# Performance work log

Hardware: AMD Instinct MI355X
Metric: run time of the kernel (lower is better)

Reference implementation:

```python
import jax, jax.numpy as jnp
import numpy as np

B, S1, S2, D1, D2 = 4, 2048, 2048, 512, 512
H, DK, DV = 8, 64, 64


def setup_inputs() -> dict:
    key = jax.random.key(0)
    ks = jax.random.split(key, 8)
    x1 = jax.random.normal(ks[0], (B, S1, D1), dtype=jnp.float32)
    x2 = jax.random.normal(ks[1], (B, S2, D2), dtype=jnp.float32)
    x3 = jax.random.normal(ks[2], (B, S2, D2), dtype=jnp.float32)
    s = 0.02
    Wq = jax.random.normal(ks[3], (D1, H * DK), dtype=jnp.float32) * s
    Wk = jax.random.normal(ks[4], (D2, H * DK), dtype=jnp.float32) * s
    Wv = jax.random.normal(ks[5], (D2, H * DV), dtype=jnp.float32) * s
    Wo = jax.random.normal(ks[6], (H * DV, D1), dtype=jnp.float32) * s
    bo = jnp.zeros((D1,), dtype=jnp.float32)
    return {"x1": x1, "x2": x2, "x3": x3, "Wq": Wq, "Wk": Wk, "Wv": Wv, "Wo": Wo, "bo": bo}


def reference(x1, x2, x3, Wq, Wk, Wv, Wo, bo):
    b, s1, _ = x1.shape
    # project to per-head q, k, v: [B, H, S, Dh]
    q = (x1 @ Wq).reshape(b, s1, H, DK).transpose(0, 2, 1, 3)
    k = (x2 @ Wk).reshape(b, x2.shape[1], H, DK).transpose(0, 2, 1, 3)
    v = (x3 @ Wv).reshape(b, x3.shape[1], H, DV).transpose(0, 2, 1, 3)
    scores = jnp.einsum('bhqd,bhkd->bhqk', q, k) / jnp.sqrt(jnp.float32(DK))
    attn = jax.nn.softmax(scores, axis=-1)
    out = jnp.einsum('bhqk,bhkd->bhqd', attn, v)  # [B, H, S1, DV]
    out = out.transpose(0, 2, 1, 3).reshape(b, s1, H * DV)
    return out @ Wo + bo
```

## Files before the change

### kernel.cpp

```cpp
#include <hip/hip_runtime.h>

typedef __attribute__((ext_vector_type(4))) float f32x4;
typedef __attribute__((ext_vector_type(16))) float f32x16;
typedef __attribute__((ext_vector_type(8))) __bf16 bf16x8;
typedef __attribute__((ext_vector_type(4))) __bf16 bf16x4;
typedef __attribute__((ext_vector_type(2))) __bf16 bf16x2;
typedef __attribute__((ext_vector_type(4))) unsigned u32x4;

#define DEVINL __device__ __forceinline__

DEVINL void gld16(const void* g, void* l) {
  __builtin_amdgcn_global_load_lds((__attribute__((address_space(1))) void*)(void*)g,
                                   (__attribute__((address_space(3))) void*)l, 16, 0, 0);
}


__global__ __launch_bounds__(256) void cvt_all(const float* x1, const float* x2, const float* x3,
                                               const float* Wq, const float* Wk, const float* Wv,
                                               const float* Wo, __bf16* o0, __bf16* o1, __bf16* o2,
                                               __bf16* WT) {
  __shared__ float t[64][65];
  const int bx = blockIdx.x;
  if (bx < 12288) {
    const int z = bx >> 12;
    const float* s = z == 0 ? x1 : z == 1 ? x2 : x3;
    __bf16* d = z == 0 ? o0 : z == 1 ? o1 : o2;
    size_t i = (size_t)(bx & 4095) * 256 + threadIdx.x;
    f32x4 v = ((const f32x4*)s)[i];
    bf16x4 o;
#pragma unroll
    for (int j = 0; j < 4; ++j) o[j] = (__bf16)v[j];
    ((bf16x4*)d)[i] = o;
  } else {
    const int l = bx - 12288;
    const int z = l >> 6;
    const float* W = z == 0 ? Wq : z == 1 ? Wk : z == 2 ? Wv : Wo;
    __bf16* D = WT + (size_t)z * 512 * 512;
    const int r0 = ((l >> 3) & 7) * 64, c0 = (l & 7) * 64;
    const int tx = threadIdx.x & 63, ty = threadIdx.x >> 6;
#pragma unroll
    for (int j = 0; j < 16; ++j)
      t[ty + j * 4][tx] = W[(size_t)(r0 + ty + j * 4) * 512 + c0 + tx];
    __syncthreads();
#pragma unroll
    for (int j = 0; j < 16; ++j)
      D[(size_t)(c0 + ty + j * 4) * 512 + r0 + tx] = (__bf16)t[tx][ty + j * 4];
  }
}


DEVINL void gemm_tile(const __bf16* A, const __bf16* Bt, int m0, int n0,
                      __bf16* As, __bf16* Bs, f32x4 acc[4][4]) {
  const int tid = threadIdx.x, lane = tid & 63, w = tid >> 6;
  const int qd = lane >> 4, r = lane & 15;
  const int wm = w & 1, wn = w >> 1;
  const char* ap[4];
  const char* bp[4];
#pragma unroll
  for (int j = 0; j < 4; ++j) {
    int c = (w * 4 + j) * 64 + lane;
    int row = c >> 3, cs = c & 7;
    int gc = cs ^ (row & 7);
    ap[j] = (const char*)A + (size_t)(m0 + row) * 1024 + gc * 16;
    bp[j] = (const char*)Bt + (size_t)(n0 + row) * 1024 + gc * 16;
  }
  int offA[4][2], offB[4][2];
#pragma unroll
  for (int t = 0; t < 4; ++t)
#pragma unroll
    for (int ks = 0; ks < 2; ++ks) {
      int m = wm * 64 + t * 16 + r;
      offA[t][ks] = m * 128 + (((ks * 4 + qd) ^ (m & 7)) * 16);
      int n = wn * 64 + t * 16 + r;
      offB[t][ks] = n * 128 + (((ks * 4 + qd) ^ (n & 7)) * 16);
    }
  char* AsC = (char*)As;
  char* BsC = (char*)Bs;
  for (int kt = 0; kt < 8; ++kt) {
    __syncthreads();
#pragma unroll
    for (int j = 0; j < 4; ++j) {
      gld16(ap[j] + kt * 128, AsC + (w * 4 + j) * 1024);
      gld16(bp[j] + kt * 128, BsC + (w * 4 + j) * 1024);
    }
    __syncthreads();
#pragma unroll
    for (int ks = 0; ks < 2; ++ks) {
      bf16x8 a[4], b[4];
#pragma unroll
      for (int t = 0; t < 4; ++t) {
        a[t] = *(const bf16x8*)(AsC + offA[t][ks]);
        b[t] = *(const bf16x8*)(BsC + offB[t][ks]);
      }
#pragma unroll
      for (int i = 0; i < 4; ++i)
#pragma unroll
        for (int j2 = 0; j2 < 4; ++j2)
          acc[i][j2] = __builtin_amdgcn_mfma_f32_16x16x32_bf16(a[i], b[j2], acc[i][j2], 0, 0, 0);
    }
  }
}

__global__ __launch_bounds__(256, 3) void gemm_proj(const __bf16* x1b, const __bf16* x2b,
                                                    const __bf16* x3b, const __bf16* WT,
                                                    __bf16* Qo, __bf16* Ko, __bf16* Vto) {
  __shared__ __align__(16) char smem[34816];
  __bf16* As = (__bf16*)smem;
  __bf16* Bs = (__bf16*)(smem + 16384);
  const int z = blockIdx.z;
  const __bf16* A = z == 0 ? x1b : z == 1 ? x2b : x3b;
  const __bf16* Bt = WT + (size_t)z * 512 * 512;
  const int l = blockIdx.x;
  const int sidx = l >> 3;
  const int m0 = ((l & 7) * 8 + (sidx >> 2)) * 128;
  const int n0 = (sidx & 3) * 128;
  f32x4 acc[4][4] = {};
  gemm_tile(A, Bt, m0, n0, As, Bs, acc);
  const int tid = threadIdx.x, lane = tid & 63, w = tid >> 6;
  const int qd = lane >> 4, r = lane & 15, wm = w & 1, wn = w >> 1;
  const int b = m0 >> 11, sbase = m0 & 2047;
  if (z == 2) {
    __syncthreads();
    char* T = smem;
#pragma unroll
    for (int mt = 0; mt < 4; ++mt)
#pragma unroll
      for (int nt = 0; nt < 4; ++nt) {
        int dv = wn * 64 + nt * 16 + r;
        int sl = wm * 64 + mt * 16 + qd * 4;
        bf16x4 p4;
#pragma unroll
        for (int g = 0; g < 4; ++g) p4[g] = (__bf16)acc[mt][nt][g];
        *(bf16x4*)(T + (size_t)dv * 272 + sl * 2) = p4;
      }
    __syncthreads();
#pragma unroll
    for (int p2 = 0; p2 < 2; ++p2) {
      int dvrow = p2 * 64 + (tid >> 2);
      int col = n0 + dvrow, h = col >> 6, d = col & 63;
      __bf16* dst = Vto + ((size_t)(b * 8 + h) * 64 + d) * 2048 + sbase + (tid & 3) * 8;
#pragma unroll
      for (int j = 0; j < 4; ++j) {
        bf16x8 vv = *(const bf16x8*)(T + (size_t)dvrow * 272 + (tid & 3) * 16 + j * 64);
        *(bf16x8*)(dst + j * 32) = vv;
      }
    }
  } else {
    const float qscale = 0.18033688f;
#pragma unroll
    for (int mt = 0; mt < 4; ++mt) {
#pragma unroll
      for (int nt = 0; nt < 4; ++nt) {
        f32x4 v = acc[mt][nt];
        if (z == 0) {
#pragma unroll
          for (int g = 0; g < 4; ++g) v[g] *= qscale;
        }
        int col = n0 + wn * 64 + nt * 16 + r;
        int h = col >> 6, d = col & 63;
        int s = sbase + wm * 64 + mt * 16 + qd * 4;
        __bf16* O = (z == 0 ? Qo : Ko) + ((size_t)(b * 8 + h) * 2048 + s) * 64 + d;
#pragma unroll
        for (int g = 0; g < 4; ++g) O[(size_t)g * 64] = (__bf16)v[g];
      }
    }
  }
}

__global__ __launch_bounds__(256, 2) void gemm_out(const __bf16* Op, const float* Lp,
                                                   const __bf16* WoT, const float* bo,
                                                   float* out) {
  __shared__ __align__(16) __bf16 As[64 * 64];
  __shared__ __align__(16) __bf16 Bs[128 * 64];
  const int tid = threadIdx.x, lane = tid & 63, w = tid >> 6;
  const int qd = lane >> 4, r = lane & 15, wm = w & 1, wn = w >> 1;
  const int id = blockIdx.x;
  const int rest = id >> 3;
  const int m0 = ((id & 7) * 16 + (rest & 15)) * 64;
  const int n0 = (rest >> 4) * 128;
  const int b8 = (m0 >> 11) * 8;
  const int sb = m0 & 2047;
  const char* bp[4];
#pragma unroll
  for (int j = 0; j < 4; ++j) {
    int c = (w * 4 + j) * 64 + lane;
    int row = c >> 3, gc = (c & 7) ^ (row & 7);
    bp[j] = (const char*)WoT + (size_t)(n0 + row) * 1024 + gc * 16;
  }
  int arow[2], ach[2];
#pragma unroll
  for (int j = 0; j < 2; ++j) {
    int c = (w * 2 + j) * 64 + lane;
    arow[j] = c >> 3;
    ach[j] = c & 7;
  }
  int offA[2][2], offB[4][2];
#pragma unroll
  for (int ks = 0; ks < 2; ++ks) {
#pragma unroll
    for (int t = 0; t < 2; ++t) {
      int m = wm * 32 + t * 16 + r;
      offA[t][ks] = m * 128 + (((ks * 4 + qd) ^ (m & 7)) * 16);
    }
#pragma unroll
    for (int t = 0; t < 4; ++t) {
      int n = wn * 64 + t * 16 + r;
      offB[t][ks] = n * 128 + (((ks * 4 + qd) ^ (n & 7)) * 16);
    }
  }
  char* AsC = (char*)As;
  char* BsC = (char*)Bs;
  bf16x8 pa0[2], pa1[2];
  float pinv[2];
  auto loadA = [&](int h) {
#pragma unroll
    for (int j = 0; j < 2; ++j) {
      size_t rr = (size_t)(b8 + h) * 2048 + sb + arow[j];
      const __bf16* p0 = Op + rr * 64 + ach[j] * 8;
      pa0[j] = *(const bf16x8*)p0;
      pa1[j] = *(const bf16x8*)(p0 + (size_t)32 * 2048 * 64);
      pinv[j] = 1.0f / (Lp[rr] + Lp[rr + 65536]);
    }
  };
  loadA(0);
  f32x4 acc[2][4] = {};
  for (int kt = 0; kt < 8; ++kt) {
    __syncthreads();
#pragma unroll
    for (int j = 0; j < 4; ++j) gld16(bp[j] + kt * 128, BsC + (w * 4 + j) * 1024);
#pragma unroll
    for (int j = 0; j < 2; ++j) {
      bf16x8 q;
#pragma unroll
      for (int k2 = 0; k2 < 8; ++k2)
        q[k2] = (__bf16)(((float)pa0[j][k2] + (float)pa1[j][k2]) * pinv[j]);
      *(bf16x8*)(AsC + arow[j] * 128 + (ach[j] ^ (arow[j] & 7)) * 16) = q;
    }
    __syncthreads();
    if (kt < 7) loadA(kt + 1);
#pragma unroll
    for (int ks = 0; ks < 2; ++ks) {
      bf16x8 a[2], b[4];
#pragma unroll
      for (int t = 0; t < 2; ++t) a[t] = *(const bf16x8*)(AsC + offA[t][ks]);
#pragma unroll
      for (int t = 0; t < 4; ++t) b[t] = *(const bf16x8*)(BsC + offB[t][ks]);
#pragma unroll
      for (int i = 0; i < 2; ++i)
#pragma unroll
        for (int j2 = 0; j2 < 4; ++j2)
          acc[i][j2] = __builtin_amdgcn_mfma_f32_16x16x32_bf16(a[i], b[j2], acc[i][j2], 0, 0, 0);
    }
  }
#pragma unroll
  for (int nt = 0; nt < 4; ++nt) {
    int col = n0 + wn * 64 + nt * 16 + r;
    float bv = bo[col];
#pragma unroll
    for (int mt = 0; mt < 2; ++mt) {
      int mg = m0 + wm * 32 + mt * 16 + qd * 4;
#pragma unroll
      for (int g = 0; g < 4; ++g) out[(size_t)(mg + g) * 512 + col] = acc[mt][nt][g] + bv;
    }
  }
}

__global__ __launch_bounds__(256, 4) void attn(const __bf16* Q, const __bf16* K,
                                               const __bf16* Vt, __bf16* Opart, float* Lp) {
  __shared__ __align__(16) __bf16 Qs[128 * 64];
  __shared__ __align__(16) __bf16 Ksd[2][64 * 64];
  __shared__ __align__(16) __bf16 Vs[64 * 64];
  const int tid = threadIdx.x, lane = tid & 63, w = tid >> 6;
  const int l31 = lane & 31, lh = lane >> 5;
  const int id = blockIdx.x;
  const int rest = id >> 3;
  const int bh = (id & 7) * 4 + (rest >> 5);
  const int kvh = (rest >> 4) & 1;
  const int q0 = (rest & 15) * 128;
  const __bf16* Qg = Q + ((size_t)bh * 2048 + q0) * 64;
  const __bf16* Kg = K + (size_t)bh * 2048 * 64;
  const __bf16* Vg = Vt + (size_t)bh * 64 * 2048;
  char* QsC = (char*)Qs;
  char* Ks0 = (char*)Ksd;
  char* Ks1 = (char*)Ksd + 8192;
  char* VsC = (char*)Vs;

  const char* Kst[2];
  const char* Vst[2];
  int ldso[2];
#pragma unroll
  for (int j = 0; j < 2; ++j) {
    int c = (w * 2 + j) * 64 + lane;
    int m = c >> 3, gc = (c & 7) ^ (m & 7);
    int ms = (m & ~12) | ((m & 4) << 1) | ((m & 8) >> 1);
    Kst[j] = (const char*)Kg + (size_t)ms * 128 + gc * 16;
    Vst[j] = (const char*)Vg + (size_t)m * 4096 + gc * 16;
    ldso[j] = (w * 2 + j) * 1024;
  }

  const int kt0 = kvh * 16;

#pragma unroll
  for (int j = 0; j < 4; ++j) {
    int c = (w * 4 + j) * 64 + lane;
    int m = c >> 3, gc = (c & 7) ^ (m & 7);
    gld16((const char*)Qg + m * 128 + gc * 16, QsC + (w * 4 + j) * 1024);
  }
#pragma unroll
  for (int j = 0; j < 2; ++j) gld16(Kst[j] + (size_t)kt0 * 8192, Ks0 + ldso[j]);
  asm volatile("s_waitcnt vmcnt(0)" ::: "memory");
  __builtin_amdgcn_sched_barrier(0);
  __builtin_amdgcn_s_barrier();
  __builtin_amdgcn_sched_barrier(0);

  const int rb = l31 * 128;
  const int he = (((lane & 7) ^ lh) << 4);

  bf16x8 qf[4];
#pragma unroll
  for (int c = 0; c < 4; ++c)
    qf[c] = *(const bf16x8*)(QsC + (w * 32 + l31) * 128 + ((c << 5) ^ he));

  bf16x8 ones;
#pragma unroll
  for (int j = 0; j < 8; ++j) ones[j] = (__bf16)1.0f;

  f32x16 oacc[2] = {};
  f32x16 lacc = {};

  auto iter = [&](int kt, int ktn, char* Kc, char* Kn) {
    gld16(Vst[0] + (size_t)kt * 128, VsC + ldso[0]);
    gld16(Vst[1] + (size_t)kt * 128, VsC + ldso[1]);
    gld16(Kst[0] + (size_t)ktn * 8192, Kn + ldso[0]);
    gld16(Kst[1] + (size_t)ktn * 8192, Kn + ldso[1]);
    __builtin_amdgcn_sched_barrier(0);

    unsigned pk[2][8];
#pragma unroll
    for (int t2 = 0; t2 < 2; ++t2) {
      f32x16 s = {};
      __builtin_amdgcn_s_setprio(1);
#pragma unroll
      for (int c = 0; c < 4; ++c) {
        bf16x8 kf = *(const bf16x8*)(Kc + t2 * 4096 + rb + ((c << 5) ^ he));
        s = __builtin_amdgcn_mfma_f32_32x32x16_bf16(kf, qf[c], s, 0, 0, 0);
      }
      __builtin_amdgcn_s_setprio(0);
#pragma unroll
      for (int i = 0; i < 8; ++i) {
        bf16x2 t;
        t[0] = (__bf16)__builtin_exp2f(s[2 * i]);
        t[1] = (__bf16)__builtin_exp2f(s[2 * i + 1]);
        pk[t2][i] = __builtin_bit_cast(unsigned, t);
      }
    }
    bf16x8 pa[4];
#pragma unroll
    for (int c = 0; c < 4; ++c) {
      u32x4 u = {pk[c >> 1][(c & 1) * 4 + 0], pk[c >> 1][(c & 1) * 4 + 1],
                 pk[c >> 1][(c & 1) * 4 + 2], pk[c >> 1][(c & 1) * 4 + 3]};
      pa[c] = __builtin_bit_cast(bf16x8, u);
    }

    asm volatile("s_waitcnt vmcnt(2)" ::: "memory");
    __builtin_amdgcn_sched_barrier(0);
    __builtin_amdgcn_s_barrier();
    __builtin_amdgcn_sched_barrier(0);

    __builtin_amdgcn_s_setprio(1);
#pragma unroll
    for (int c = 0; c < 4; ++c) {
      lacc = __builtin_amdgcn_mfma_f32_32x32x16_bf16(pa[c], ones, lacc, 0, 0, 0);
#pragma unroll
      for (int dvt = 0; dvt < 2; ++dvt) {
        bf16x8 vf = *(const bf16x8*)(VsC + dvt * 4096 + rb + ((c << 5) ^ he));
        oacc[dvt] = __builtin_amdgcn_mfma_f32_32x32x16_bf16(pa[c], vf, oacc[dvt], 0, 0, 0);
      }
    }
    __builtin_amdgcn_s_setprio(0);

    asm volatile("s_waitcnt vmcnt(0)" ::: "memory");
    __builtin_amdgcn_sched_barrier(0);
    __builtin_amdgcn_s_barrier();
    __builtin_amdgcn_sched_barrier(0);
  };

#pragma unroll 1
  for (int kt = kt0; kt < kt0 + 16; kt += 2) {
    iter(kt, kt + 1, Ks0, Ks1);
    int kt2 = (kt + 2 < kt0 + 16) ? kt + 2 : kt + 1;
    iter(kt + 1, kt2, Ks1, Ks0);
  }

  const size_t pbase = (size_t)(kvh * 32 + bh) * 2048;
  if (l31 == 0) {
#pragma unroll
    for (int g = 0; g < 16; ++g)
      Lp[pbase + q0 + w * 32 + (g & 3) + 8 * (g >> 2) + 4 * lh] = lacc[g];
  }
  __bf16* Ob0 = Opart + pbase * 64;
#pragma unroll
  for (int dvt = 0; dvt < 2; ++dvt) {
#pragma unroll
    for (int g = 0; g < 16; ++g) {
      int s = q0 + w * 32 + (g & 3) + 8 * (g >> 2) + 4 * lh;
      Ob0[(size_t)s * 64 + dvt * 32 + l31] = (__bf16)oacc[dvt][g];
    }
  }
}


extern "C" void kernel_launch(void* const* d_in, const int* in_sizes, int n_in,
                              void* d_out, int out_size, void* d_ws, size_t ws_size,
                              hipStream_t stream) {
  const float* x1 = (const float*)d_in[0];
  const float* x2 = (const float*)d_in[1];
  const float* x3 = (const float*)d_in[2];
  const float* Wq = (const float*)d_in[3];
  const float* Wk = (const float*)d_in[4];
  const float* Wv = (const float*)d_in[5];
  const float* Wo = (const float*)d_in[6];
  const float* bo = (const float*)d_in[7];
  float* out = (float*)d_out;
  char* ws = (char*)d_ws;
  const size_t MB = 1ull << 20;
  __bf16* x1b = (__bf16*)(ws);
  __bf16* x2b = (__bf16*)(ws + 8 * MB);
  __bf16* x3b = (__bf16*)(ws + 16 * MB);
  __bf16* WT = (__bf16*)(ws + 24 * MB);
  __bf16* Qb = (__bf16*)(ws + 26 * MB);
  __bf16* Kb = (__bf16*)(ws + 34 * MB);
  __bf16* Vtb = (__bf16*)(ws + 42 * MB);
  __bf16* Opart = (__bf16*)(ws + 58 * MB);
  float* Lp = (float*)(ws + 74 * MB);

  cvt_all<<<dim3(12544), 256, 0, stream>>>(x1, x2, x3, Wq, Wk, Wv, Wo, x1b, x2b, x3b, WT);
  gemm_proj<<<dim3(256, 1, 3), 256, 0, stream>>>(x1b, x2b, x3b, WT, Qb, Kb, Vtb);
  attn<<<dim3(1024), 256, 0, stream>>>(Qb, Kb, Vtb, Opart, Lp);
  gemm_out<<<dim3(512), 256, 0, stream>>>(Opart, Lp, WT + 3ull * 512 * 512, bo, out);
}
```

Before: 194.3 us.

## Software-pipeline attention loop: overlap next QK and softmax with current PV

```diff
diff --git a/kernel.cpp b/kernel.cpp
--- a/kernel.cpp
+++ b/kernel.cpp
@@ -277,49 +277,50 @@
   const int bh = (id & 7) * 4 + (rest >> 5);
   const int kvh = (rest >> 4) & 1;
   const int q0 = (rest & 15) * 128;
-  const __bf16* Qg = Q + ((size_t)bh * 2048 + q0) * 64;
-  const __bf16* Kg = K + (size_t)bh * 2048 * 64;
-  const __bf16* Vg = Vt + (size_t)bh * 64 * 2048;
+  const char* QgC = (const char*)(Q + ((size_t)bh * 2048 + q0) * 64);
+  const char* KgC = (const char*)(K + (size_t)bh * 2048 * 64);
+  const char* VgC = (const char*)(Vt + (size_t)bh * 64 * 2048);
   char* QsC = (char*)Qs;
-  char* Ks0 = (char*)Ksd;
-  char* Ks1 = (char*)Ksd + 8192;
   char* VsC = (char*)Vs;
-
-  const char* Kst[2];
-  const char* Vst[2];
-  int ldso[2];
+  char* Kc = (char*)Ksd;
+  char* Kn = (char*)Ksd + 8192;
+
+  int koff[2], voff[2], ldso[2];
 #pragma unroll
   for (int j = 0; j < 2; ++j) {
     int c = (w * 2 + j) * 64 + lane;
     int m = c >> 3, gc = (c & 7) ^ (m & 7);
     int ms = (m & ~12) | ((m & 4) << 1) | ((m & 8) >> 1);
-    Kst[j] = (const char*)Kg + (size_t)ms * 128 + gc * 16;
-    Vst[j] = (const char*)Vg + (size_t)m * 4096 + gc * 16;
+    koff[j] = ms * 128 + gc * 16;
+    voff[j] = m * 4096 + gc * 16;
     ldso[j] = (w * 2 + j) * 1024;
   }
 
   const int kt0 = kvh * 16;
+  const size_t kb = (size_t)kt0 * 8192;
+  const size_t vb = (size_t)kt0 * 128;
 
 #pragma unroll
   for (int j = 0; j < 4; ++j) {
     int c = (w * 4 + j) * 64 + lane;
     int m = c >> 3, gc = (c & 7) ^ (m & 7);
-    gld16((const char*)Qg + m * 128 + gc * 16, QsC + (w * 4 + j) * 1024);
-  }
-#pragma unroll
-  for (int j = 0; j < 2; ++j) gld16(Kst[j] + (size_t)kt0 * 8192, Ks0 + ldso[j]);
-  asm volatile("s_waitcnt vmcnt(0)" ::: "memory");
+    gld16(QgC + m * 128 + gc * 16, QsC + (w * 4 + j) * 1024);
+  }
+  gld16(KgC + kb + koff[0], Kc + ldso[0]);
+  gld16(KgC + kb + koff[1], Kc + ldso[1]);
+  gld16(VgC + vb + voff[0], VsC + ldso[0]);
+  gld16(VgC + vb + voff[1], VsC + ldso[1]);
+  gld16(KgC + kb + 8192 + koff[0], Kn + ldso[0]);
+  gld16(KgC + kb + 8192 + koff[1], Kn + ldso[1]);
+  __builtin_amdgcn_sched_barrier(0);
+  asm volatile("s_waitcnt vmcnt(2)" ::: "memory");
   __builtin_amdgcn_sched_barrier(0);
   __builtin_amdgcn_s_barrier();
   __builtin_amdgcn_sched_barrier(0);
 
   const int rb = l31 * 128;
   const int he = (((lane & 7) ^ lh) << 4);
-
-  bf16x8 qf[4];
-#pragma unroll
-  for (int c = 0; c < 4; ++c)
-    qf[c] = *(const bf16x8*)(QsC + (w * 32 + l31) * 128 + ((c << 5) ^ he));
+  const int qrow = (w * 32 + l31) * 128;
 
   bf16x8 ones;
 #pragma unroll
@@ -327,69 +328,93 @@
 
   f32x16 oacc[2] = {};
   f32x16 lacc = {};
-
-  auto iter = [&](int kt, int ktn, char* Kc, char* Kn) {
-    gld16(Vst[0] + (size_t)kt * 128, VsC + ldso[0]);
-    gld16(Vst[1] + (size_t)kt * 128, VsC + ldso[1]);
-    gld16(Kst[0] + (size_t)ktn * 8192, Kn + ldso[0]);
-    gld16(Kst[1] + (size_t)ktn * 8192, Kn + ldso[1]);
-    __builtin_amdgcn_sched_barrier(0);
-
-    unsigned pk[2][8];
-#pragma unroll
-    for (int t2 = 0; t2 < 2; ++t2) {
-      f32x16 s = {};
-      __builtin_amdgcn_s_setprio(1);
-#pragma unroll
-      for (int c = 0; c < 4; ++c) {
-        bf16x8 kf = *(const bf16x8*)(Kc + t2 * 4096 + rb + ((c << 5) ^ he));
-        s = __builtin_amdgcn_mfma_f32_32x32x16_bf16(kf, qf[c], s, 0, 0, 0);
-      }
-      __builtin_amdgcn_s_setprio(0);
-#pragma unroll
-      for (int i = 0; i < 8; ++i) {
-        bf16x2 t;
-        t[0] = (__bf16)__builtin_exp2f(s[2 * i]);
-        t[1] = (__bf16)__builtin_exp2f(s[2 * i + 1]);
-        pk[t2][i] = __builtin_bit_cast(unsigned, t);
-      }
-    }
-    bf16x8 pa[4];
+  bf16x8 pa[4];
+
+  auto smhalf = [&](const f32x16& s, bf16x8& pa0, bf16x8& pa1) {
+    unsigned wds[8];
+#pragma unroll
+    for (int i = 0; i < 8; ++i) {
+      bf16x2 t;
+      t[0] = (__bf16)__builtin_exp2f(s[2 * i]);
+      t[1] = (__bf16)__builtin_exp2f(s[2 * i + 1]);
+      wds[i] = __builtin_bit_cast(unsigned, t);
+    }
+    pa0 = __builtin_bit_cast(bf16x8, (u32x4){wds[0], wds[1], wds[2], wds[3]});
+    pa1 = __builtin_bit_cast(bf16x8, (u32x4){wds[4], wds[5], wds[6], wds[7]});
+  };
+  auto qkchain = [&](const char* Kb, int half, const bf16x8 qf[4]) {
+    f32x16 s = {};
 #pragma unroll
     for (int c = 0; c < 4; ++c) {
-      u32x4 u = {pk[c >> 1][(c & 1) * 4 + 0], pk[c >> 1][(c & 1) * 4 + 1],
-                 pk[c >> 1][(c & 1) * 4 + 2], pk[c >> 1][(c & 1) * 4 + 3]};
-      pa[c] = __builtin_bit_cast(bf16x8, u);
-    }
-
-    asm volatile("s_waitcnt vmcnt(2)" ::: "memory");
-    __builtin_amdgcn_sched_barrier(0);
-    __builtin_amdgcn_s_barrier();
-    __builtin_amdgcn_sched_barrier(0);
-
+      bf16x8 kf = *(const bf16x8*)(Kb + half * 4096 + rb + ((c << 5) ^ he));
+      s = __builtin_amdgcn_mfma_f32_32x32x16_bf16(kf, qf[c], s, 0, 0, 0);
+    }
+    return s;
+  };
+
+  {
+    bf16x8 qf[4];
+#pragma unroll
+    for (int c = 0; c < 4; ++c) qf[c] = *(const bf16x8*)(QsC + qrow + ((c << 5) ^ he));
+    f32x16 s0 = qkchain(Kc, 0, qf);
+    f32x16 s1 = qkchain(Kc, 1, qf);
+    smhalf(s0, pa[0], pa[1]);
+    smhalf(s1, pa[2], pa[3]);
+  }
+  __builtin_amdgcn_sched_barrier(0);
+  asm volatile("s_waitcnt vmcnt(0)" ::: "memory");
+  __builtin_amdgcn_sched_barrier(0);
+  __builtin_amdgcn_s_barrier();
+  __builtin_amdgcn_sched_barrier(0);
+
+#pragma unroll 1
+  for (int t = 0; t < 15; ++t) {
     __builtin_amdgcn_s_setprio(1);
 #pragma unroll
     for (int c = 0; c < 4; ++c) {
       lacc = __builtin_amdgcn_mfma_f32_32x32x16_bf16(pa[c], ones, lacc, 0, 0, 0);
-#pragma unroll
-      for (int dvt = 0; dvt < 2; ++dvt) {
-        bf16x8 vf = *(const bf16x8*)(VsC + dvt * 4096 + rb + ((c << 5) ^ he));
-        oacc[dvt] = __builtin_amdgcn_mfma_f32_32x32x16_bf16(pa[c], vf, oacc[dvt], 0, 0, 0);
-      }
-    }
+      bf16x8 vf0 = *(const bf16x8*)(VsC + rb + ((c << 5) ^ he));
+      oacc[0] = __builtin_amdgcn_mfma_f32_32x32x16_bf16(pa[c], vf0, oacc[0], 0, 0, 0);
+      bf16x8 vf1 = *(const bf16x8*)(VsC + 4096 + rb + ((c << 5) ^ he));
+      oacc[1] = __builtin_amdgcn_mfma_f32_32x32x16_bf16(pa[c], vf1, oacc[1], 0, 0, 0);
+    }
+    bf16x8 qf[4];
+#pragma unroll
+    for (int c = 0; c < 4; ++c) qf[c] = *(const bf16x8*)(QsC + qrow + ((c << 5) ^ he));
+    f32x16 s0 = qkchain(Kn, 0, qf);
+    f32x16 s1 = qkchain(Kn, 1, qf);
+    smhalf(s0, pa[0], pa[1]);
     __builtin_amdgcn_s_setprio(0);
-
+    __builtin_amdgcn_sched_barrier(0);
+    __builtin_amdgcn_s_barrier();
+    __builtin_amdgcn_sched_barrier(0);
+
+    gld16(VgC + vb + (size_t)(t + 1) * 128 + voff[0], VsC + ldso[0]);
+    gld16(VgC + vb + (size_t)(t + 1) * 128 + voff[1], VsC + ldso[1]);
+    if (t < 14) {
+      gld16(KgC + kb + (size_t)(t + 2) * 8192 + koff[0], Kc + ldso[0]);
+      gld16(KgC + kb + (size_t)(t + 2) * 8192 + koff[1], Kc + ldso[1]);
+    }
+    __builtin_amdgcn_sched_barrier(0);
+    smhalf(s1, pa[2], pa[3]);
+    __builtin_amdgcn_sched_barrier(0);
     asm volatile("s_waitcnt vmcnt(0)" ::: "memory");
     __builtin_amdgcn_sched_barrier(0);
     __builtin_amdgcn_s_barrier();
     __builtin_amdgcn_sched_barrier(0);
-  };
-
-#pragma unroll 1
-  for (int kt = kt0; kt < kt0 + 16; kt += 2) {
-    iter(kt, kt + 1, Ks0, Ks1);
-    int kt2 = (kt + 2 < kt0 + 16) ? kt + 2 : kt + 1;
-    iter(kt + 1, kt2, Ks1, Ks0);
+
+    char* tmp = Kc;
+    Kc = Kn;
+    Kn = tmp;
+  }
+
+#pragma unroll
+  for (int c = 0; c < 4; ++c) {
+    lacc = __builtin_amdgcn_mfma_f32_32x32x16_bf16(pa[c], ones, lacc, 0, 0, 0);
+    bf16x8 vf0 = *(const bf16x8*)(VsC + rb + ((c << 5) ^ he));
+    oacc[0] = __builtin_amdgcn_mfma_f32_32x32x16_bf16(pa[c], vf0, oacc[0], 0, 0, 0);
+    bf16x8 vf1 = *(const bf16x8*)(VsC + 4096 + rb + ((c << 5) ^ he));
+    oacc[1] = __builtin_amdgcn_mfma_f32_32x32x16_bf16(pa[c], vf1, oacc[1], 0, 0, 0);
   }
 
   const size_t pbase = (size_t)(kvh * 32 + bh) * 2048;
```

Result: faster. 188.8 us (-2.8%).
